# Kernel optimization log

Hardware: AMD Instinct MI355X
Metric: run time of the kernel (lower is better)

## Reference

```python
import jax, jax.numpy as jnp
import numpy as np

D_MODEL = 768; D_KV = 64; H = 12; D_FF = 3072; L = 2
TP = 4; SP = 16; MT = 16; MS = 4
MASK_RATE = 0.2; EPS = 1e-6
B = 256; T = 64; F = 64
ST = (T // TP) * (F // SP)  # 64 tokens


def ln(x, s, b):
    mu = jnp.mean(x, -1, keepdims=True)
    var = jnp.mean(jnp.square(x - mu), -1, keepdims=True)
    return (x - mu) * jax.lax.rsqrt(var + EPS) * s + b


def mha(x, Wq, bq, Wk, bk, Wv, bv, Wo, bo):
    Bz, S, D = x.shape
    q = (x @ Wq + bq).reshape(Bz, S, H, D_KV)
    k = (x @ Wk + bk).reshape(Bz, S, H, D_KV)
    v = (x @ Wv + bv).reshape(Bz, S, H, D_KV)
    scores = jnp.einsum('bqhd,bkhd->bhqk', q, k) * (D_KV ** -0.5)
    attn = jax.nn.softmax(scores, axis=-1)
    o = jnp.einsum('bhqk,bkhd->bqhd', attn, v).reshape(Bz, S, H * D_KV)
    return o @ Wo + bo


def setup_inputs():
    key = jax.random.key(0)
    ks = jax.random.split(key, 16)
    s = 0.02
    nrm = lambda k, shp: jax.random.normal(k, shp, jnp.float32) * s
    return {
        'inputs': jax.random.normal(ks[0], (B, T, F, 1), jnp.float32),
        'randomness': jax.random.uniform(ks[1], (B * ST, 3), jnp.float32),
        'perm': jax.random.permutation(ks[2], B * ST),
        'conv_w': nrm(ks[3], (TP, SP, 1, D_MODEL)), 'conv_b': jnp.zeros((D_MODEL,)),
        'temp_embd': nrm(ks[4], (MT, D_MODEL)), 'spec_embd': nrm(ks[5], (MS, D_MODEL)),
        'pos_ln_s': jnp.ones((D_MODEL,)), 'pos_ln_b': jnp.zeros((D_MODEL,)),
        'mask_tok': nrm(ks[6], (D_MODEL,)), 'agg_tok': nrm(ks[7], (D_MODEL,)),
        'Wq': nrm(ks[8], (L, D_MODEL, H * D_KV)), 'bq': jnp.zeros((L, H * D_KV)),
        'Wk': nrm(ks[9], (L, D_MODEL, H * D_KV)), 'bk': jnp.zeros((L, H * D_KV)),
        'Wv': nrm(ks[10], (L, D_MODEL, H * D_KV)), 'bv': jnp.zeros((L, H * D_KV)),
        'Wo': nrm(ks[11], (L, H * D_KV, D_MODEL)), 'bo': jnp.zeros((L, D_MODEL)),
        'ln1_s': jnp.ones((L, D_MODEL)), 'ln1_b': jnp.zeros((L, D_MODEL)),
        'W1': nrm(ks[12], (L, D_MODEL, D_FF)), 'b1': jnp.zeros((L, D_FF)),
        'W2': nrm(ks[13], (L, D_FF, D_MODEL)), 'b2': jnp.zeros((L, D_MODEL)),
        'ln2_s': jnp.ones((L, D_MODEL)), 'ln2_b': jnp.zeros((L, D_MODEL)),
    }


def reference(inputs, randomness, perm, conv_w, conv_b, temp_embd, spec_embd,
              pos_ln_s, pos_ln_b, mask_tok, agg_tok, Wq, bq, Wk, bk, Wv, bv,
              Wo, bo, ln1_s, ln1_b, W1, b1, W2, b2, ln2_s, ln2_b):
    # Conv2D patchify: [B, T, F, 1] -> [B, T/4, F/16, d_model]
    x = jax.lax.conv_general_dilated(
        inputs, conv_w, (TP, SP), 'VALID',
        dimension_numbers=('NHWC', 'HWIO', 'NHWC')) + conv_b
    Bz, Tt, Ss, D = x.shape
    e = x.reshape(Bz, Tt * Ss, D)  # token embeddings [B, 64, 768]
    # Vectorized BERT-style random masking (replaces the per-element sparse-scatter loop)
    sel = randomness[:, 0] <= MASK_RATE
    m = (sel & (randomness[:, 1] <= 0.8)).astype(e.dtype).reshape(Bz, Tt * Ss)
    rnd = (sel & (randomness[:, 1] > 0.8) & (randomness[:, 2] <= 0.5)).astype(e.dtype).reshape(Bz, Tt * Ss)
    shuffled = jax.lax.stop_gradient(e.reshape(-1, D))[perm].reshape(Bz, Tt * Ss, D)
    me = e * (1.0 - m - rnd)[..., None] + mask_tok * m[..., None] + shuffled * rnd[..., None]
    # Spectro-temporal position embeddings + LN
    pos = (temp_embd[:Tt, None, :] + spec_embd[None, :Ss, :]).reshape(Tt * Ss, D)
    h = ln(me + pos, pos_ln_s, pos_ln_b)
    # Prepend AGG token
    h = jnp.concatenate([jnp.broadcast_to(agg_tok, (Bz, 1, D)), h], axis=1)
    # Post-norm transformer encoder
    for l in range(L):
        a = mha(h, Wq[l], bq[l], Wk[l], bk[l], Wv[l], bv[l], Wo[l], bo[l])
        h = ln(h + a, ln1_s[l], ln1_b[l])
        f = jax.nn.gelu(h @ W1[l] + b1[l], approximate=False) @ W2[l] + b2[l]
        h = ln(h + f, ln2_s[l], ln2_b[l])
    return h  # last_hidden_states [B, 65, 768]; aggregated=h[:,0], predictions=h[:,1:]
```

## Files before the change

kernel.cpp:

```cpp
#include <hip/hip_runtime.h>
#include <hip/hip_bf16.h>
#include <math.h>

using bf16 = __hip_bfloat16;
typedef __bf16 bf16x8v __attribute__((ext_vector_type(8)));
typedef float f32x4 __attribute__((ext_vector_type(4)));
typedef unsigned short ushort4v __attribute__((ext_vector_type(4)));
typedef unsigned short ushort8v __attribute__((ext_vector_type(8)));

__device__ __forceinline__ float b2f(bf16 x) { return __bfloat162float(x); }
__device__ __forceinline__ bf16 f2b(float x) { return __float2bfloat16(x); }

__device__ __forceinline__ void gload_lds16(const void* g, void* l) {
  __builtin_amdgcn_global_load_lds(
      (__attribute__((address_space(1))) void*)(void*)g,
      (__attribute__((address_space(3))) void*)l, 16, 0, 0);
}

__device__ __forceinline__ float block_sum(float v, float* buf) {
  #pragma unroll
  for (int off = 32; off > 0; off >>= 1) v += __shfl_xor(v, off);
  __syncthreads();
  if ((threadIdx.x & 63) == 0) buf[threadIdx.x >> 6] = v;
  __syncthreads();
  return buf[0] + buf[1] + buf[2] + buf[3];
}

__global__ __launch_bounds__(256) void transpose_kernel(
    const float* __restrict__ in, bf16* __restrict__ out, int K, int N) {
  __shared__ float tile[32][33];
  const int nbx = N >> 5;
  const int bx = blockIdx.x % nbx, by = blockIdx.x / nbx;
  const int tx = threadIdx.x & 31, ty = threadIdx.x >> 5;
  #pragma unroll
  for (int i = 0; i < 4; ++i) {
    const int r = by * 32 + ty + i * 8;
    tile[ty + i * 8][tx] = in[(size_t)r * N + bx * 32 + tx];
  }
  __syncthreads();
  #pragma unroll
  for (int i = 0; i < 4; ++i) {
    const int r = bx * 32 + ty + i * 8;
    out[(size_t)r * K + by * 32 + tx] = f2b(tile[tx][ty + i * 8]);
  }
}

__global__ __launch_bounds__(256) void biasqkv_kernel(
    const float* __restrict__ bq, const float* __restrict__ bk,
    const float* __restrict__ bv, float* __restrict__ out) {
  const int i = blockIdx.x * 256 + threadIdx.x;
  if (i >= 2 * 2304) return;
  const int l = i / 2304, n = i % 2304;
  float v = (n < 768) ? bq[l * 768 + n]
          : (n < 1536) ? bk[l * 768 + n - 768] : bv[l * 768 + n - 1536];
  out[i] = v;
}

__global__ __launch_bounds__(256) void patchify_kernel(
    const float* __restrict__ in, const float* __restrict__ w,
    const float* __restrict__ cb, bf16* __restrict__ e) {
  __shared__ float patch[8][64];
  const int tid = threadIdx.x;
  const int tok0 = blockIdx.x * 8;
  for (int idx = tid; idx < 512; idx += 256) {
    const int t = idx >> 6, p = idx & 63;
    const int tok = tok0 + t;
    const int b = tok >> 6, t2 = tok & 63, tt = t2 >> 2, ss = t2 & 3;
    const int kt = p >> 4, kf = p & 15;
    patch[t][p] = in[((size_t)b * 64 + tt * 4 + kt) * 64 + ss * 16 + kf];
  }
  __syncthreads();
  for (int i = 0; i < 3; ++i) {
    const int d = tid + i * 256;
    const float cbv = cb[d];
    float acc[8];
    #pragma unroll
    for (int t = 0; t < 8; ++t) acc[t] = cbv;
    for (int p = 0; p < 64; ++p) {
      const float wv = w[p * 768 + d];
      #pragma unroll
      for (int t = 0; t < 8; ++t) acc[t] += patch[t][p] * wv;
    }
    #pragma unroll
    for (int t = 0; t < 8; ++t) e[(size_t)(tok0 + t) * 768 + d] = f2b(acc[t]);
  }
}

__global__ __launch_bounds__(256) void embed_kernel(
    const bf16* __restrict__ e, const float* __restrict__ randomness,
    const int* __restrict__ perm, const float* __restrict__ temp_embd,
    const float* __restrict__ spec_embd, const float* __restrict__ pls,
    const float* __restrict__ plb, const float* __restrict__ mask_tok,
    const float* __restrict__ agg_tok, bf16* __restrict__ h) {
  __shared__ float rbuf[4];
  const int row = blockIdx.x;
  const int b = row / 65, s = row % 65;
  const int tid = threadIdx.x;
  const size_t ob = (size_t)row * 768;
  if (s == 0) {
    #pragma unroll
    for (int i = 0; i < 3; ++i) { const int d = tid + i * 256; h[ob + d] = f2b(agg_tok[d]); }
    return;
  }
  const int tok = s - 1;
  const int gt = b * 64 + tok;
  const float r0 = randomness[gt * 3 + 0];
  const float r1 = randomness[gt * 3 + 1];
  const float r2 = randomness[gt * 3 + 2];
  const bool selb = (r0 <= 0.2f);
  const bool mflag = selb && (r1 <= 0.8f);
  const bool rflag = selb && (r1 > 0.8f) && (r2 <= 0.5f);
  const int src = rflag ? perm[gt] : gt;
  const int tt = tok >> 2, ss2 = tok & 3;
  float v[3]; float sum = 0.f;
  #pragma unroll
  for (int i = 0; i < 3; ++i) {
    const int d = tid + i * 256;
    const float ev = mflag ? mask_tok[d] : b2f(e[(size_t)src * 768 + d]);
    v[i] = ev + temp_embd[tt * 768 + d] + spec_embd[ss2 * 768 + d];
    sum += v[i];
  }
  const float mu = block_sum(sum, rbuf) * (1.f / 768.f);
  float q = 0.f;
  #pragma unroll
  for (int i = 0; i < 3; ++i) { const float t = v[i] - mu; q += t * t; }
  const float rstd = rsqrtf(block_sum(q, rbuf) * (1.f / 768.f) + 1e-6f);
  #pragma unroll
  for (int i = 0; i < 3; ++i) {
    const int d = tid + i * 256;
    h[ob + d] = f2b((v[i] - mu) * rstd * pls[d] + plb[d]);
  }
}

template <int F32OUT>
__global__ __launch_bounds__(256) void resln_kernel(
    const bf16* __restrict__ x, const bf16* __restrict__ y,
    const float* __restrict__ sc, const float* __restrict__ bi,
    void* __restrict__ outp) {
  __shared__ float rbuf[4];
  const int tid = threadIdx.x;
  const size_t base = (size_t)blockIdx.x * 768;
  float v[3]; float s = 0.f;
  #pragma unroll
  for (int i = 0; i < 3; ++i) {
    const int d = tid + i * 256;
    v[i] = b2f(x[base + d]) + b2f(y[base + d]);
    s += v[i];
  }
  const float mu = block_sum(s, rbuf) * (1.f / 768.f);
  float q = 0.f;
  #pragma unroll
  for (int i = 0; i < 3; ++i) { const float t = v[i] - mu; q += t * t; }
  const float rstd = rsqrtf(block_sum(q, rbuf) * (1.f / 768.f) + 1e-6f);
  #pragma unroll
  for (int i = 0; i < 3; ++i) {
    const int d = tid + i * 256;
    const float o = (v[i] - mu) * rstd * sc[d] + bi[d];
    if (F32OUT) ((float*)outp)[base + d] = o;
    else        ((bf16*)outp)[base + d] = f2b(o);
  }
}

template <int ACT>
__global__ __launch_bounds__(512, 2) void gemmkh_kernel(
    const unsigned short* __restrict__ A, const unsigned short* __restrict__ BT,
    const float* __restrict__ bias, bf16* __restrict__ C, int N, int K, int nbn) {
  __shared__ __align__(16) char smem[131072];

  const int nwg = gridDim.x;
  const int orig = blockIdx.x;
  const int q8 = nwg >> 3, r8 = nwg & 7;
  const int xcd = orig & 7, lin = orig >> 3;
  const int bid = (xcd < r8 ? xcd * (q8 + 1) : r8 * (q8 + 1) + (xcd - r8) * q8) + lin;
  const int bm = bid / nbn, bn = bid % nbn;

  const int tid = threadIdx.x;
  const int w = tid >> 6, lane = tid & 63;
  const int wrow = w >> 2, wcol = w & 3;
  const int frow = lane & 15;
  const int cg = lane >> 4;

  const size_t Kb = (size_t)K * 2;
  const int srow = lane >> 2;
  const int srcCB = (((lane & 3) ^ ((lane >> 3) & 3)) << 4);
  const char* gA = (const char*)A + ((size_t)bm * 256) * Kb;
  const char* gB = (const char*)BT + ((size_t)bn * 256) * Kb;

  f32x4 acc[8][4];
  #pragma unroll
  for (int i = 0; i < 8; ++i)
    #pragma unroll
    for (int j = 0; j < 4; ++j) acc[i][j] = f32x4{0.f, 0.f, 0.f, 0.f};

  auto stagePair = [&](int t, int h) {
    char* slot = smem + (size_t)(t & 1) * 65536;
    const size_t colb = (size_t)t * 128 + h * 64 + srcCB;
    #pragma unroll
    for (int j = 0; j < 2; ++j) {
      const int r = w * 32 + j * 16 + srow;
      gload_lds16(gA + (size_t)r * Kb + colb, slot + h * 16384 + w * 2048 + j * 1024);
      gload_lds16(gB + (size_t)r * Kb + colb, slot + 32768 + h * 16384 + w * 2048 + j * 1024);
    }
  };

  auto phase = [&](int t, int h) {
    const char* slot = smem + (size_t)(t & 1) * 65536;
    bf16x8v bb[4], aa[8];
    #pragma unroll
    for (int n = 0; n < 4; ++n) {
      const int row = wcol * 64 + n * 16 + frow;
      bb[n] = *(const bf16x8v*)(slot + 32768 + h * 16384 + row * 64 +
                                ((cg ^ ((row >> 1) & 3)) << 4));
    }
    #pragma unroll
    for (int m = 0; m < 8; ++m) {
      const int row = wrow * 128 + m * 16 + frow;
      aa[m] = *(const bf16x8v*)(slot + h * 16384 + row * 64 +
                                ((cg ^ ((row >> 1) & 3)) << 4));
    }
    __builtin_amdgcn_s_setprio(1);
    #pragma unroll
    for (int m = 0; m < 8; ++m)
      #pragma unroll
      for (int n = 0; n < 4; ++n)
        acc[m][n] = __builtin_amdgcn_mfma_f32_16x16x32_bf16(aa[m], bb[n], acc[m][n], 0, 0, 0);
    __builtin_amdgcn_s_setprio(0);
  };

  const int T = K >> 6;
  stagePair(0, 0);
  stagePair(0, 1);

  for (int t = 0; t < T - 1; ++t) {
    stagePair(t + 1, 0);
    asm volatile("s_waitcnt vmcnt(8)" ::: "memory");
    __builtin_amdgcn_s_barrier();
    __builtin_amdgcn_sched_barrier(0);
    phase(t, 0);
    stagePair(t + 1, 1);
    asm volatile("s_waitcnt vmcnt(8)" ::: "memory");
    __builtin_amdgcn_s_barrier();
    __builtin_amdgcn_sched_barrier(0);
    phase(t, 1);
  }
  asm volatile("s_waitcnt vmcnt(4)" ::: "memory");
  __builtin_amdgcn_s_barrier();
  __builtin_amdgcn_sched_barrier(0);
  phase(T - 1, 0);
  asm volatile("s_waitcnt vmcnt(0)" ::: "memory");
  __builtin_amdgcn_s_barrier();
  __builtin_amdgcn_sched_barrier(0);
  phase(T - 1, 1);
  __syncthreads();

  bf16* cbuf = (bf16*)smem;
  float bias4[4];
  #pragma unroll
  for (int n = 0; n < 4; ++n) bias4[n] = bias[bn * 256 + wcol * 64 + n * 16 + frow];
  const int rgrp = (lane >> 4) << 2;
  #pragma unroll
  for (int half = 0; half < 2; ++half) {
    if (wrow == half) {
      #pragma unroll
      for (int mf = 0; mf < 8; ++mf)
        #pragma unroll
        for (int n = 0; n < 4; ++n) {
          const int col = wcol * 64 + n * 16 + frow;
          #pragma unroll
          for (int r = 0; r < 4; ++r) {
            float v = acc[mf][n][r] + bias4[n];
            if (ACT == 1) v = 0.5f * v * (1.0f + erff(v * 0.70710678f));
            cbuf[(mf * 16 + rgrp + r) * 264 + col] = f2b(v);
          }
        }
    }
    __syncthreads();
    #pragma unroll
    for (int jj = 0; jj < 8; ++jj) {
      const int idx = tid + jj * 512;
      const int rowl = idx >> 5, c = idx & 31;
      const ushort8v val = *(const ushort8v*)(cbuf + rowl * 264 + c * 8);
      *(ushort8v*)(C + ((size_t)(bm * 256 + half * 128 + rowl)) * N + (size_t)bn * 256 + c * 8) = val;
    }
    __syncthreads();
  }
}

__global__ __launch_bounds__(320) void attn_mfma_kernel(
    const bf16* __restrict__ qkv, bf16* __restrict__ ctx) {
  __shared__ __align__(16) bf16 sK[80][72];
  __shared__ __align__(16) bf16 sVt[64][104];
  __shared__ __align__(16) bf16 sP[5][16][104];
  const int b = blockIdx.x / 12, h = blockIdx.x % 12;
  const int tid = threadIdx.x;
  const int wave = tid >> 6, lane = tid & 63;
  const size_t base = ((size_t)b * 65) * 2304 + (size_t)h * 64;
  const bf16 bzero = f2b(0.f);

  for (int idx = tid; idx < 65 * 16; idx += 320) {
    const int row = idx >> 4, d4 = (idx & 15) * 4;
    const ushort4v kv = *(const ushort4v*)(qkv + base + (size_t)row * 2304 + 768 + d4);
    const ushort4v vv = *(const ushort4v*)(qkv + base + (size_t)row * 2304 + 1536 + d4);
    *(ushort4v*)&sK[row][d4] = kv;
    #pragma unroll
    for (int j = 0; j < 4; ++j) ((unsigned short*)&sVt[d4 + j][row])[0] = vv[j];
  }
  for (int idx = tid; idx < 15 * 16; idx += 320) {
    const int row = 65 + (idx >> 4), d4 = (idx & 15) * 4;
    *(ushort4v*)&sK[row][d4] = ushort4v{0, 0, 0, 0};
  }
  for (int idx = tid; idx < 64 * 31; idx += 320) {
    const int d = idx / 31, c = 65 + (idx % 31);
    sVt[d][c] = bzero;
  }
  __syncthreads();

  const int frow = lane & 15;
  const int koff = (lane >> 4) * 8;
  const int row0 = wave * 16;
  const int qrow = (row0 + frow > 64) ? 64 : (row0 + frow);
  const bf16* qptr = qkv + base + (size_t)qrow * 2304;
  const bf16x8v aq0 = *(const bf16x8v*)(qptr + koff);
  const bf16x8v aq1 = *(const bf16x8v*)(qptr + 32 + koff);

  const f32x4 z4 = {0.f, 0.f, 0.f, 0.f};
  f32x4 sacc[5];
  #pragma unroll
  for (int n = 0; n < 5; ++n) sacc[n] = z4;
  #pragma unroll
  for (int n = 0; n < 5; ++n) {
    const bf16x8v b0 = *(const bf16x8v*)&sK[n * 16 + frow][koff];
    const bf16x8v b1 = *(const bf16x8v*)&sK[n * 16 + frow][32 + koff];
    sacc[n] = __builtin_amdgcn_mfma_f32_16x16x32_bf16(aq0, b0, sacc[n], 0, 0, 0);
    sacc[n] = __builtin_amdgcn_mfma_f32_16x16x32_bf16(aq1, b1, sacc[n], 0, 0, 0);
  }

  #pragma unroll
  for (int r = 0; r < 4; ++r) {
    const int prow = ((lane >> 4) << 2) + r;
    float v[5];
    float mx = -1e30f;
    #pragma unroll
    for (int n = 0; n < 5; ++n) {
      const int col = n * 16 + frow;
      v[n] = (col < 65) ? sacc[n][r] * 0.125f : -1e30f;
      mx = fmaxf(mx, v[n]);
    }
    #pragma unroll
    for (int off = 1; off < 16; off <<= 1) mx = fmaxf(mx, __shfl_xor(mx, off));
    float sum = 0.f;
    #pragma unroll
    for (int n = 0; n < 5; ++n) { v[n] = __expf(v[n] - mx); sum += v[n]; }
    #pragma unroll
    for (int off = 1; off < 16; off <<= 1) sum += __shfl_xor(sum, off);
    const float inv = 1.f / sum;
    #pragma unroll
    for (int n = 0; n < 5; ++n)
      sP[wave][prow][n * 16 + frow] = f2b(v[n] * inv);
    sP[wave][prow][80 + frow] = bzero;
  }

  f32x4 oacc[4];
  #pragma unroll
  for (int n = 0; n < 4; ++n) oacc[n] = z4;
  #pragma unroll
  for (int kk = 0; kk < 3; ++kk) {
    const bf16x8v ap = *(const bf16x8v*)&sP[wave][frow][kk * 32 + koff];
    #pragma unroll
    for (int n = 0; n < 4; ++n) {
      const bf16x8v bv = *(const bf16x8v*)&sVt[n * 16 + frow][kk * 32 + koff];
      oacc[n] = __builtin_amdgcn_mfma_f32_16x16x32_bf16(ap, bv, oacc[n], 0, 0, 0);
    }
  }

  #pragma unroll
  for (int r = 0; r < 4; ++r) {
    const int row = row0 + ((lane >> 4) << 2) + r;
    if (row < 65) {
      bf16* op = ctx + ((size_t)b * 65 + row) * 768 + (size_t)h * 64 + frow;
      #pragma unroll
      for (int n = 0; n < 4; ++n) op[n * 16] = f2b(oacc[n][r]);
    }
  }
}

extern "C" void kernel_launch(void* const* d_in, const int* in_sizes, int n_in,
                              void* d_out, int out_size, void* d_ws, size_t ws_size,
                              hipStream_t stream) {
  (void)in_sizes; (void)n_in; (void)out_size; (void)ws_size;
  const float* inputs     = (const float*)d_in[0];
  const float* randomness = (const float*)d_in[1];
  const int*   perm       = (const int*)d_in[2];
  const float* conv_w     = (const float*)d_in[3];
  const float* conv_b     = (const float*)d_in[4];
  const float* temp_embd  = (const float*)d_in[5];
  const float* spec_embd  = (const float*)d_in[6];
  const float* pos_ln_s   = (const float*)d_in[7];
  const float* pos_ln_b   = (const float*)d_in[8];
  const float* mask_tok   = (const float*)d_in[9];
  const float* agg_tok    = (const float*)d_in[10];
  const float* Wq = (const float*)d_in[11]; const float* bq = (const float*)d_in[12];
  const float* Wk = (const float*)d_in[13]; const float* bk = (const float*)d_in[14];
  const float* Wv = (const float*)d_in[15]; const float* bv = (const float*)d_in[16];
  const float* Wo = (const float*)d_in[17]; const float* bo = (const float*)d_in[18];
  const float* ln1_s = (const float*)d_in[19]; const float* ln1_b = (const float*)d_in[20];
  const float* W1 = (const float*)d_in[21]; const float* b1 = (const float*)d_in[22];
  const float* W2 = (const float*)d_in[23]; const float* b2 = (const float*)d_in[24];
  const float* ln2_s = (const float*)d_in[25]; const float* ln2_b = (const float*)d_in[26];

  char* wsb = (char*)d_ws;
  size_t off = 0;
  auto carve = [&](size_t bytes) { char* p = wsb + off; off = (off + bytes + 255) & ~(size_t)255; return p; };
  bf16* wqkvT = (bf16*)carve((size_t)2 * 2304 * 768 * 2);
  bf16* woT   = (bf16*)carve((size_t)2 * 768 * 768 * 2);
  bf16* w1T   = (bf16*)carve((size_t)2 * 3072 * 768 * 2);
  bf16* w2T   = (bf16*)carve((size_t)2 * 768 * 3072 * 2);
  float* bqkv = (float*)carve((size_t)2 * 2304 * 4);
  bf16* ebuf  = (bf16*)carve((size_t)16640 * 768 * 2);
  bf16* hbuf  = (bf16*)carve((size_t)16640 * 768 * 2);
  bf16* qkvb  = (bf16*)carve((size_t)16640 * 2304 * 2);
  bf16* ctxb  = (bf16*)carve((size_t)16640 * 768 * 2);
  bf16* tmpb  = ebuf;
  bf16* midb  = qkvb;

  const dim3 blk(256);
  for (int l = 0; l < 2; ++l) {
    transpose_kernel<<<576, blk, 0, stream>>>(Wq + (size_t)l * 768 * 768, wqkvT + (size_t)l * 2304 * 768, 768, 768);
    transpose_kernel<<<576, blk, 0, stream>>>(Wk + (size_t)l * 768 * 768, wqkvT + (size_t)l * 2304 * 768 + 768 * 768, 768, 768);
    transpose_kernel<<<576, blk, 0, stream>>>(Wv + (size_t)l * 768 * 768, wqkvT + (size_t)l * 2304 * 768 + 2 * 768 * 768, 768, 768);
    transpose_kernel<<<576, blk, 0, stream>>>(Wo + (size_t)l * 768 * 768, woT + (size_t)l * 768 * 768, 768, 768);
    transpose_kernel<<<2304, blk, 0, stream>>>(W1 + (size_t)l * 768 * 3072, w1T + (size_t)l * 3072 * 768, 768, 3072);
    transpose_kernel<<<2304, blk, 0, stream>>>(W2 + (size_t)l * 3072 * 768, w2T + (size_t)l * 768 * 3072, 3072, 768);
  }
  biasqkv_kernel<<<18, blk, 0, stream>>>(bq, bk, bv, bqkv);
  patchify_kernel<<<2048, blk, 0, stream>>>(inputs, conv_w, conv_b, ebuf);
  embed_kernel<<<16640, blk, 0, stream>>>(ebuf, randomness, perm, temp_embd, spec_embd,
                                          pos_ln_s, pos_ln_b, mask_tok, agg_tok, hbuf);
  for (int l = 0; l < 2; ++l) {
    gemmkh_kernel<0><<<65 * 9, dim3(512), 0, stream>>>(
        (const unsigned short*)hbuf, (const unsigned short*)(wqkvT + (size_t)l * 2304 * 768),
        bqkv + l * 2304, qkvb, 2304, 768, 9);
    attn_mfma_kernel<<<256 * 12, dim3(320), 0, stream>>>(qkvb, ctxb);
    gemmkh_kernel<0><<<65 * 3, dim3(512), 0, stream>>>(
        (const unsigned short*)ctxb, (const unsigned short*)(woT + (size_t)l * 768 * 768),
        bo + l * 768, tmpb, 768, 768, 3);
    resln_kernel<0><<<16640, blk, 0, stream>>>(hbuf, tmpb, ln1_s + l * 768, ln1_b + l * 768, hbuf);
    gemmkh_kernel<1><<<65 * 12, dim3(512), 0, stream>>>(
        (const unsigned short*)hbuf, (const unsigned short*)(w1T + (size_t)l * 3072 * 768),
        b1 + l * 3072, midb, 3072, 768, 12);
    gemmkh_kernel<0><<<65 * 3, dim3(512), 0, stream>>>(
        (const unsigned short*)midb, (const unsigned short*)(w2T + (size_t)l * 768 * 3072),
        b2 + l * 768, tmpb, 768, 3072, 3);
    if (l == 1)
      resln_kernel<1><<<16640, blk, 0, stream>>>(hbuf, tmpb, ln2_s + l * 768, ln2_b + l * 768, d_out);
    else
      resln_kernel<0><<<16640, blk, 0, stream>>>(hbuf, tmpb, ln2_s + l * 768, ln2_b + l * 768, hbuf);
  }
}
```

Baseline: 1.013 ms.

## Use triple-buffered K=32 GEMM pipeline and narrower N tiles for D_MODEL-output GEMMs

Replaces the double-buffered two-half-stage GEMM main loop with a three-slot ring buffer over K-steps of 32, prefetching two steps ahead behind a single barrier per step. It also adds a template option for 128-wide N tiles and uses it for the Wo and W2 projections, which doubles their grid from 195 to 390 workgroups. The aim is better latency hiding and better CU occupancy on the N=768 GEMMs. The cost is more barriers per unit of K, smaller per-barrier compute and lower arithmetic intensity for the narrow tiles.

```diff
diff --git a/kernel.cpp b/kernel.cpp
--- a/kernel.cpp
+++ b/kernel.cpp
@@ -161,11 +161,20 @@
   }
 }
 
-template <int ACT>
-__global__ __launch_bounds__(512, 2) void gemmkh_kernel(
+template <int WN, int ACT>
+__global__ __launch_bounds__(512, 2) void gemmp2_kernel(
     const unsigned short* __restrict__ A, const unsigned short* __restrict__ BT,
     const float* __restrict__ bias, bf16* __restrict__ C, int N, int K, int nbn) {
-  __shared__ __align__(16) char smem[131072];
+  constexpr int BN = 64 * WN;
+  constexpr int ABYTES = 256 * 64;
+  constexpr int BBYTES = BN * 64;
+  constexpr int SLOT = ABYTES + BBYTES;
+  constexpr int LPT = (256 + BN) / 128;
+  constexpr int MF = (WN == 4) ? 8 : 4;
+  constexpr int PADC = BN + 8;
+  constexpr int EPIB = (WN == 4) ? 128 * PADC * 2 : 256 * PADC * 2;
+  constexpr int SMEMB = (3 * SLOT > EPIB) ? 3 * SLOT : EPIB;
+  __shared__ __align__(16) char smem[SMEMB];
 
   const int nwg = gridDim.x;
   const int orig = blockIdx.x;
@@ -176,113 +185,131 @@
 
   const int tid = threadIdx.x;
   const int w = tid >> 6, lane = tid & 63;
-  const int wrow = w >> 2, wcol = w & 3;
+  const int wrow = (WN == 4) ? (w >> 2) : (w >> 1);
+  const int wcol = (WN == 4) ? (w & 3) : (w & 1);
   const int frow = lane & 15;
   const int cg = lane >> 4;
 
   const size_t Kb = (size_t)K * 2;
-  const int srow = lane >> 2;
+  const int g_lr = lane >> 2;
   const int srcCB = (((lane & 3) ^ ((lane >> 3) & 3)) << 4);
   const char* gA = (const char*)A + ((size_t)bm * 256) * Kb;
-  const char* gB = (const char*)BT + ((size_t)bn * 256) * Kb;
-
-  f32x4 acc[8][4];
-  #pragma unroll
-  for (int i = 0; i < 8; ++i)
+  const char* gB = (const char*)BT + ((size_t)bn * BN) * Kb;
+
+  f32x4 acc[MF][4];
+  #pragma unroll
+  for (int i = 0; i < MF; ++i)
     #pragma unroll
     for (int j = 0; j < 4; ++j) acc[i][j] = f32x4{0.f, 0.f, 0.f, 0.f};
 
-  auto stagePair = [&](int t, int h) {
-    char* slot = smem + (size_t)(t & 1) * 65536;
-    const size_t colb = (size_t)t * 128 + h * 64 + srcCB;
-    #pragma unroll
-    for (int j = 0; j < 2; ++j) {
-      const int r = w * 32 + j * 16 + srow;
-      gload_lds16(gA + (size_t)r * Kb + colb, slot + h * 16384 + w * 2048 + j * 1024);
-      gload_lds16(gB + (size_t)r * Kb + colb, slot + 32768 + h * 16384 + w * 2048 + j * 1024);
+  auto stage = [&](int t) {
+    char* slot = smem + (t % 3) * SLOT;
+    const size_t kb = (size_t)t * 64 + srcCB;
+    #pragma unroll
+    for (int g = 0; g < 2; ++g) {
+      const int r = g * 128 + w * 16 + g_lr;
+      gload_lds16(gA + (size_t)r * Kb + kb, slot + (g * 128 + w * 16) * 64);
+    }
+    #pragma unroll
+    for (int g = 0; g < LPT - 2; ++g) {
+      const int r = g * 128 + w * 16 + g_lr;
+      gload_lds16(gB + (size_t)r * Kb + kb, slot + ABYTES + (g * 128 + w * 16) * 64);
     }
   };
 
-  auto phase = [&](int t, int h) {
-    const char* slot = smem + (size_t)(t & 1) * 65536;
-    bf16x8v bb[4], aa[8];
+  auto compute = [&](int t) {
+    const char* slot = smem + (t % 3) * SLOT;
+    bf16x8v bb[4], aa[MF];
     #pragma unroll
     for (int n = 0; n < 4; ++n) {
       const int row = wcol * 64 + n * 16 + frow;
-      bb[n] = *(const bf16x8v*)(slot + 32768 + h * 16384 + row * 64 +
-                                ((cg ^ ((row >> 1) & 3)) << 4));
-    }
-    #pragma unroll
-    for (int m = 0; m < 8; ++m) {
-      const int row = wrow * 128 + m * 16 + frow;
-      aa[m] = *(const bf16x8v*)(slot + h * 16384 + row * 64 +
-                                ((cg ^ ((row >> 1) & 3)) << 4));
+      bb[n] = *(const bf16x8v*)(slot + ABYTES + row * 64 + ((cg ^ ((row >> 1) & 3)) << 4));
+    }
+    #pragma unroll
+    for (int m = 0; m < MF; ++m) {
+      const int row = wrow * (MF * 16) + m * 16 + frow;
+      aa[m] = *(const bf16x8v*)(slot + row * 64 + ((cg ^ ((row >> 1) & 3)) << 4));
     }
     __builtin_amdgcn_s_setprio(1);
     #pragma unroll
-    for (int m = 0; m < 8; ++m)
+    for (int m = 0; m < MF; ++m)
       #pragma unroll
       for (int n = 0; n < 4; ++n)
         acc[m][n] = __builtin_amdgcn_mfma_f32_16x16x32_bf16(aa[m], bb[n], acc[m][n], 0, 0, 0);
     __builtin_amdgcn_s_setprio(0);
   };
 
-  const int T = K >> 6;
-  stagePair(0, 0);
-  stagePair(0, 1);
-
-  for (int t = 0; t < T - 1; ++t) {
-    stagePair(t + 1, 0);
-    asm volatile("s_waitcnt vmcnt(8)" ::: "memory");
+  const int T = K >> 5;
+  stage(0);
+  stage(1);
+  for (int t = 0; t < T; ++t) {
+    if (t + 1 < T) {
+      if constexpr (WN == 4) asm volatile("s_waitcnt vmcnt(4)" ::: "memory");
+      else                   asm volatile("s_waitcnt vmcnt(3)" ::: "memory");
+    } else {
+      asm volatile("s_waitcnt vmcnt(0)" ::: "memory");
+    }
+    asm volatile("s_waitcnt lgkmcnt(0)" ::: "memory");
     __builtin_amdgcn_s_barrier();
     __builtin_amdgcn_sched_barrier(0);
-    phase(t, 0);
-    stagePair(t + 1, 1);
-    asm volatile("s_waitcnt vmcnt(8)" ::: "memory");
-    __builtin_amdgcn_s_barrier();
-    __builtin_amdgcn_sched_barrier(0);
-    phase(t, 1);
-  }
-  asm volatile("s_waitcnt vmcnt(4)" ::: "memory");
-  __builtin_amdgcn_s_barrier();
-  __builtin_amdgcn_sched_barrier(0);
-  phase(T - 1, 0);
-  asm volatile("s_waitcnt vmcnt(0)" ::: "memory");
-  __builtin_amdgcn_s_barrier();
-  __builtin_amdgcn_sched_barrier(0);
-  phase(T - 1, 1);
+    if (t + 2 < T) stage(t + 2);
+    compute(t);
+  }
   __syncthreads();
 
   bf16* cbuf = (bf16*)smem;
   float bias4[4];
   #pragma unroll
-  for (int n = 0; n < 4; ++n) bias4[n] = bias[bn * 256 + wcol * 64 + n * 16 + frow];
+  for (int n = 0; n < 4; ++n) bias4[n] = bias[bn * BN + wcol * 64 + n * 16 + frow];
   const int rgrp = (lane >> 4) << 2;
-  #pragma unroll
-  for (int half = 0; half < 2; ++half) {
-    if (wrow == half) {
+  if constexpr (WN == 4) {
+    #pragma unroll
+    for (int half = 0; half < 2; ++half) {
+      if (wrow == half) {
+        #pragma unroll
+        for (int mf = 0; mf < MF; ++mf)
+          #pragma unroll
+          for (int n = 0; n < 4; ++n) {
+            const int col = wcol * 64 + n * 16 + frow;
+            #pragma unroll
+            for (int r = 0; r < 4; ++r) {
+              float v = acc[mf][n][r] + bias4[n];
+              if (ACT == 1) v = 0.5f * v * (1.0f + erff(v * 0.70710678f));
+              cbuf[(mf * 16 + rgrp + r) * PADC + col] = f2b(v);
+            }
+          }
+      }
+      __syncthreads();
       #pragma unroll
-      for (int mf = 0; mf < 8; ++mf)
+      for (int jj = 0; jj < 8; ++jj) {
+        const int idx = tid + jj * 512;
+        const int rowl = idx >> 5, c = idx & 31;
+        const ushort8v val = *(const ushort8v*)(cbuf + rowl * PADC + c * 8);
+        *(ushort8v*)(C + ((size_t)(bm * 256 + half * 128 + rowl)) * N + (size_t)bn * BN + c * 8) = val;
+      }
+      __syncthreads();
+    }
+  } else {
+    #pragma unroll
+    for (int mf = 0; mf < MF; ++mf)
+      #pragma unroll
+      for (int n = 0; n < 4; ++n) {
+        const int col = wcol * 64 + n * 16 + frow;
         #pragma unroll
-        for (int n = 0; n < 4; ++n) {
-          const int col = wcol * 64 + n * 16 + frow;
-          #pragma unroll
-          for (int r = 0; r < 4; ++r) {
-            float v = acc[mf][n][r] + bias4[n];
-            if (ACT == 1) v = 0.5f * v * (1.0f + erff(v * 0.70710678f));
-            cbuf[(mf * 16 + rgrp + r) * 264 + col] = f2b(v);
-          }
+        for (int r = 0; r < 4; ++r) {
+          float v = acc[mf][n][r] + bias4[n];
+          if (ACT == 1) v = 0.5f * v * (1.0f + erff(v * 0.70710678f));
+          cbuf[(wrow * 64 + mf * 16 + rgrp + r) * PADC + col] = f2b(v);
         }
-    }
+      }
     __syncthreads();
     #pragma unroll
     for (int jj = 0; jj < 8; ++jj) {
       const int idx = tid + jj * 512;
-      const int rowl = idx >> 5, c = idx & 31;
-      const ushort8v val = *(const ushort8v*)(cbuf + rowl * 264 + c * 8);
-      *(ushort8v*)(C + ((size_t)(bm * 256 + half * 128 + rowl)) * N + (size_t)bn * 256 + c * 8) = val;
-    }
-    __syncthreads();
+      const int rowl = idx >> 4, c = idx & 15;
+      const ushort8v val = *(const ushort8v*)(cbuf + rowl * PADC + c * 8);
+      *(ushort8v*)(C + ((size_t)(bm * 256 + rowl)) * N + (size_t)bn * BN + c * 8) = val;
+    }
   }
 }
 
@@ -437,20 +464,20 @@
   embed_kernel<<<16640, blk, 0, stream>>>(ebuf, randomness, perm, temp_embd, spec_embd,
                                           pos_ln_s, pos_ln_b, mask_tok, agg_tok, hbuf);
   for (int l = 0; l < 2; ++l) {
-    gemmkh_kernel<0><<<65 * 9, dim3(512), 0, stream>>>(
+    gemmp2_kernel<4, 0><<<65 * 9, dim3(512), 0, stream>>>(
         (const unsigned short*)hbuf, (const unsigned short*)(wqkvT + (size_t)l * 2304 * 768),
         bqkv + l * 2304, qkvb, 2304, 768, 9);
     attn_mfma_kernel<<<256 * 12, dim3(320), 0, stream>>>(qkvb, ctxb);
-    gemmkh_kernel<0><<<65 * 3, dim3(512), 0, stream>>>(
+    gemmp2_kernel<2, 0><<<65 * 6, dim3(512), 0, stream>>>(
         (const unsigned short*)ctxb, (const unsigned short*)(woT + (size_t)l * 768 * 768),
-        bo + l * 768, tmpb, 768, 768, 3);
+        bo + l * 768, tmpb, 768, 768, 6);
     resln_kernel<0><<<16640, blk, 0, stream>>>(hbuf, tmpb, ln1_s + l * 768, ln1_b + l * 768, hbuf);
-    gemmkh_kernel<1><<<65 * 12, dim3(512), 0, stream>>>(
+    gemmp2_kernel<4, 1><<<65 * 12, dim3(512), 0, stream>>>(
         (const unsigned short*)hbuf, (const unsigned short*)(w1T + (size_t)l * 3072 * 768),
         b1 + l * 3072, midb, 3072, 768, 12);
-    gemmkh_kernel<0><<<65 * 3, dim3(512), 0, stream>>>(
+    gemmp2_kernel<2, 0><<<65 * 6, dim3(512), 0, stream>>>(
         (const unsigned short*)midb, (const unsigned short*)(w2T + (size_t)l * 768 * 3072),
-        b2 + l * 768, tmpb, 768, 3072, 3);
+        b2 + l * 768, tmpb, 768, 3072, 6);
     if (l == 1)
       resln_kernel<1><<<16640, blk, 0, stream>>>(hbuf, tmpb, ln2_s + l * 768, ln2_b + l * 768, d_out);
     else
```

Result: slower. 1.054 ms (+4.0%).

## Shrink GEMM tile to 256x128 with simple double buffer; merge weight transposes

Applied to the files above, without the earlier changes.

Replaces the 256x256 GEMM tile and its split-K pipelined staging with a 256x128 tile that stages one 32-wide K slice per iteration into a small double buffer. The kernel now uses 48KB of LDS and launch bounds of 4, so more workgroups can be resident and the grid is twice as large, which helps with tail and occupancy on small-N GEMMs. The cost is less reuse per tile, more barriers per K step, and giving up the hand-tuned vmcnt overlap. Separately, the twelve weight-transpose launches are merged into one kernel to cut launch overhead.

```diff
diff --git a/kernel.cpp b/kernel.cpp
--- a/kernel.cpp
+++ b/kernel.cpp
@@ -26,22 +26,44 @@
   return buf[0] + buf[1] + buf[2] + buf[3];
 }
 
-__global__ __launch_bounds__(256) void transpose_kernel(
-    const float* __restrict__ in, bf16* __restrict__ out, int K, int N) {
+__global__ __launch_bounds__(256) void transpose_all_kernel(
+    const float* __restrict__ Wq, const float* __restrict__ Wk,
+    const float* __restrict__ Wv, const float* __restrict__ Wo,
+    const float* __restrict__ W1, const float* __restrict__ W2,
+    bf16* __restrict__ wqkvT, bf16* __restrict__ woT,
+    bf16* __restrict__ w1T, bf16* __restrict__ w2T) {
   __shared__ float tile[32][33];
+  const int tb = blockIdx.x;
+  const float* src; bf16* dst; int K, N, t;
+  if (tb < 4608) {
+    const int job = tb / 576; t = tb % 576;
+    const int l = job >> 2, c = job & 3;
+    src = (c == 0 ? Wq : c == 1 ? Wk : c == 2 ? Wv : Wo) + (size_t)l * 768 * 768;
+    dst = (c < 3) ? (wqkvT + (size_t)l * 2304 * 768 + (size_t)c * 768 * 768)
+                  : (woT + (size_t)l * 768 * 768);
+    K = 768; N = 768;
+  } else if (tb < 9216) {
+    const int r = tb - 4608; const int l = r / 2304; t = r % 2304;
+    src = W1 + (size_t)l * 768 * 3072; dst = w1T + (size_t)l * 3072 * 768;
+    K = 768; N = 3072;
+  } else {
+    const int r = tb - 9216; const int l = r / 2304; t = r % 2304;
+    src = W2 + (size_t)l * 3072 * 768; dst = w2T + (size_t)l * 768 * 3072;
+    K = 3072; N = 768;
+  }
   const int nbx = N >> 5;
-  const int bx = blockIdx.x % nbx, by = blockIdx.x / nbx;
+  const int bx = t % nbx, by = t / nbx;
   const int tx = threadIdx.x & 31, ty = threadIdx.x >> 5;
   #pragma unroll
   for (int i = 0; i < 4; ++i) {
     const int r = by * 32 + ty + i * 8;
-    tile[ty + i * 8][tx] = in[(size_t)r * N + bx * 32 + tx];
+    tile[ty + i * 8][tx] = src[(size_t)r * N + bx * 32 + tx];
   }
   __syncthreads();
   #pragma unroll
   for (int i = 0; i < 4; ++i) {
     const int r = bx * 32 + ty + i * 8;
-    out[(size_t)r * K + by * 32 + tx] = f2b(tile[tx][ty + i * 8]);
+    dst[(size_t)r * K + by * 32 + tx] = f2b(tile[tx][ty + i * 8]);
   }
 }
 
@@ -162,10 +184,13 @@
 }
 
 template <int ACT>
-__global__ __launch_bounds__(512, 2) void gemmkh_kernel(
+__global__ __launch_bounds__(512, 4) void gemm2b_kernel(
     const unsigned short* __restrict__ A, const unsigned short* __restrict__ BT,
     const float* __restrict__ bias, bf16* __restrict__ C, int N, int K, int nbn) {
-  __shared__ __align__(16) char smem[131072];
+  constexpr int ABYTES = 256 * 64;
+  constexpr int BBYTES = 128 * 64;
+  constexpr int SLOT = ABYTES + BBYTES;
+  __shared__ __align__(16) char smem[2 * SLOT];
 
   const int nwg = gridDim.x;
   const int orig = blockIdx.x;
@@ -176,93 +201,79 @@
 
   const int tid = threadIdx.x;
   const int w = tid >> 6, lane = tid & 63;
-  const int wrow = w >> 2, wcol = w & 3;
+  const int wrow = w >> 1, wcol = w & 1;
   const int frow = lane & 15;
   const int cg = lane >> 4;
 
   const size_t Kb = (size_t)K * 2;
-  const int srow = lane >> 2;
+  const int g_lr = lane >> 2;
   const int srcCB = (((lane & 3) ^ ((lane >> 3) & 3)) << 4);
   const char* gA = (const char*)A + ((size_t)bm * 256) * Kb;
-  const char* gB = (const char*)BT + ((size_t)bn * 256) * Kb;
-
-  f32x4 acc[8][4];
-  #pragma unroll
-  for (int i = 0; i < 8; ++i)
+  const char* gB = (const char*)BT + ((size_t)bn * 128) * Kb;
+
+  f32x4 acc[4][4];
+  #pragma unroll
+  for (int i = 0; i < 4; ++i)
     #pragma unroll
     for (int j = 0; j < 4; ++j) acc[i][j] = f32x4{0.f, 0.f, 0.f, 0.f};
 
-  auto stagePair = [&](int t, int h) {
-    char* slot = smem + (size_t)(t & 1) * 65536;
-    const size_t colb = (size_t)t * 128 + h * 64 + srcCB;
+  auto stage = [&](int t, int slotIdx) {
+    char* slot = smem + slotIdx * SLOT;
+    const size_t kb = (size_t)t * 64 + srcCB;
     #pragma unroll
     for (int j = 0; j < 2; ++j) {
-      const int r = w * 32 + j * 16 + srow;
-      gload_lds16(gA + (size_t)r * Kb + colb, slot + h * 16384 + w * 2048 + j * 1024);
-      gload_lds16(gB + (size_t)r * Kb + colb, slot + 32768 + h * 16384 + w * 2048 + j * 1024);
+      const int r0 = w * 32 + j * 16;
+      gload_lds16(gA + (size_t)(r0 + g_lr) * Kb + kb, slot + r0 * 64);
+    }
+    {
+      const int r0 = w * 16;
+      gload_lds16(gB + (size_t)(r0 + g_lr) * Kb + kb, slot + ABYTES + r0 * 64);
     }
   };
 
-  auto phase = [&](int t, int h) {
-    const char* slot = smem + (size_t)(t & 1) * 65536;
-    bf16x8v bb[4], aa[8];
+  auto compute = [&](int slotIdx) {
+    const char* slot = smem + slotIdx * SLOT;
+    bf16x8v aa[4], bb[4];
     #pragma unroll
     for (int n = 0; n < 4; ++n) {
       const int row = wcol * 64 + n * 16 + frow;
-      bb[n] = *(const bf16x8v*)(slot + 32768 + h * 16384 + row * 64 +
-                                ((cg ^ ((row >> 1) & 3)) << 4));
-    }
-    #pragma unroll
-    for (int m = 0; m < 8; ++m) {
-      const int row = wrow * 128 + m * 16 + frow;
-      aa[m] = *(const bf16x8v*)(slot + h * 16384 + row * 64 +
-                                ((cg ^ ((row >> 1) & 3)) << 4));
+      bb[n] = *(const bf16x8v*)(slot + ABYTES + row * 64 + ((cg ^ ((row >> 1) & 3)) << 4));
+    }
+    #pragma unroll
+    for (int m = 0; m < 4; ++m) {
+      const int row = wrow * 64 + m * 16 + frow;
+      aa[m] = *(const bf16x8v*)(slot + row * 64 + ((cg ^ ((row >> 1) & 3)) << 4));
     }
     __builtin_amdgcn_s_setprio(1);
     #pragma unroll
-    for (int m = 0; m < 8; ++m)
+    for (int m = 0; m < 4; ++m)
       #pragma unroll
       for (int n = 0; n < 4; ++n)
         acc[m][n] = __builtin_amdgcn_mfma_f32_16x16x32_bf16(aa[m], bb[n], acc[m][n], 0, 0, 0);
     __builtin_amdgcn_s_setprio(0);
   };
 
-  const int T = K >> 6;
-  stagePair(0, 0);
-  stagePair(0, 1);
-
-  for (int t = 0; t < T - 1; ++t) {
-    stagePair(t + 1, 0);
-    asm volatile("s_waitcnt vmcnt(8)" ::: "memory");
-    __builtin_amdgcn_s_barrier();
-    __builtin_amdgcn_sched_barrier(0);
-    phase(t, 0);
-    stagePair(t + 1, 1);
-    asm volatile("s_waitcnt vmcnt(8)" ::: "memory");
-    __builtin_amdgcn_s_barrier();
-    __builtin_amdgcn_sched_barrier(0);
-    phase(t, 1);
-  }
-  asm volatile("s_waitcnt vmcnt(4)" ::: "memory");
-  __builtin_amdgcn_s_barrier();
-  __builtin_amdgcn_sched_barrier(0);
-  phase(T - 1, 0);
-  asm volatile("s_waitcnt vmcnt(0)" ::: "memory");
-  __builtin_amdgcn_s_barrier();
-  __builtin_amdgcn_sched_barrier(0);
-  phase(T - 1, 1);
-  __syncthreads();
+  const int T = K >> 5;
+  stage(0, 0);
+  __syncthreads();
+  int cur = 0;
+  for (int t = 0; t < T; ++t) {
+    if (t + 1 < T) stage(t + 1, cur ^ 1);
+    compute(cur);
+    __syncthreads();
+    cur ^= 1;
+  }
 
   bf16* cbuf = (bf16*)smem;
   float bias4[4];
   #pragma unroll
-  for (int n = 0; n < 4; ++n) bias4[n] = bias[bn * 256 + wcol * 64 + n * 16 + frow];
+  for (int n = 0; n < 4; ++n) bias4[n] = bias[bn * 128 + wcol * 64 + n * 16 + frow];
   const int rgrp = (lane >> 4) << 2;
   #pragma unroll
-  for (int half = 0; half < 2; ++half) {
-    if (wrow == half) {
+  for (int qtr = 0; qtr < 4; ++qtr) {
+    if (wrow == qtr) {
       #pragma unroll
-      for (int mf = 0; mf < 8; ++mf)
+      for (int mf = 0; mf < 4; ++mf)
         #pragma unroll
         for (int n = 0; n < 4; ++n) {
           const int col = wcol * 64 + n * 16 + frow;
@@ -270,17 +281,17 @@
           for (int r = 0; r < 4; ++r) {
             float v = acc[mf][n][r] + bias4[n];
             if (ACT == 1) v = 0.5f * v * (1.0f + erff(v * 0.70710678f));
-            cbuf[(mf * 16 + rgrp + r) * 264 + col] = f2b(v);
+            cbuf[(mf * 16 + rgrp + r) * 136 + col] = f2b(v);
           }
         }
     }
     __syncthreads();
     #pragma unroll
-    for (int jj = 0; jj < 8; ++jj) {
+    for (int jj = 0; jj < 2; ++jj) {
       const int idx = tid + jj * 512;
-      const int rowl = idx >> 5, c = idx & 31;
-      const ushort8v val = *(const ushort8v*)(cbuf + rowl * 264 + c * 8);
-      *(ushort8v*)(C + ((size_t)(bm * 256 + half * 128 + rowl)) * N + (size_t)bn * 256 + c * 8) = val;
+      const int rowl = idx >> 4, c = idx & 15;
+      const ushort8v val = *(const ushort8v*)(cbuf + rowl * 136 + c * 8);
+      *(ushort8v*)(C + ((size_t)(bm * 256 + qtr * 64 + rowl)) * N + (size_t)bn * 128 + c * 8) = val;
     }
     __syncthreads();
   }
@@ -424,33 +435,27 @@
   bf16* midb  = qkvb;
 
   const dim3 blk(256);
-  for (int l = 0; l < 2; ++l) {
-    transpose_kernel<<<576, blk, 0, stream>>>(Wq + (size_t)l * 768 * 768, wqkvT + (size_t)l * 2304 * 768, 768, 768);
-    transpose_kernel<<<576, blk, 0, stream>>>(Wk + (size_t)l * 768 * 768, wqkvT + (size_t)l * 2304 * 768 + 768 * 768, 768, 768);
-    transpose_kernel<<<576, blk, 0, stream>>>(Wv + (size_t)l * 768 * 768, wqkvT + (size_t)l * 2304 * 768 + 2 * 768 * 768, 768, 768);
-    transpose_kernel<<<576, blk, 0, stream>>>(Wo + (size_t)l * 768 * 768, woT + (size_t)l * 768 * 768, 768, 768);
-    transpose_kernel<<<2304, blk, 0, stream>>>(W1 + (size_t)l * 768 * 3072, w1T + (size_t)l * 3072 * 768, 768, 3072);
-    transpose_kernel<<<2304, blk, 0, stream>>>(W2 + (size_t)l * 3072 * 768, w2T + (size_t)l * 768 * 3072, 3072, 768);
-  }
+  transpose_all_kernel<<<13824, blk, 0, stream>>>(Wq, Wk, Wv, Wo, W1, W2,
+                                                  wqkvT, woT, w1T, w2T);
   biasqkv_kernel<<<18, blk, 0, stream>>>(bq, bk, bv, bqkv);
   patchify_kernel<<<2048, blk, 0, stream>>>(inputs, conv_w, conv_b, ebuf);
   embed_kernel<<<16640, blk, 0, stream>>>(ebuf, randomness, perm, temp_embd, spec_embd,
                                           pos_ln_s, pos_ln_b, mask_tok, agg_tok, hbuf);
   for (int l = 0; l < 2; ++l) {
-    gemmkh_kernel<0><<<65 * 9, dim3(512), 0, stream>>>(
+    gemm2b_kernel<0><<<65 * 18, dim3(512), 0, stream>>>(
         (const unsigned short*)hbuf, (const unsigned short*)(wqkvT + (size_t)l * 2304 * 768),
-        bqkv + l * 2304, qkvb, 2304, 768, 9);
+        bqkv + l * 2304, qkvb, 2304, 768, 18);
     attn_mfma_kernel<<<256 * 12, dim3(320), 0, stream>>>(qkvb, ctxb);
-    gemmkh_kernel<0><<<65 * 3, dim3(512), 0, stream>>>(
+    gemm2b_kernel<0><<<65 * 6, dim3(512), 0, stream>>>(
         (const unsigned short*)ctxb, (const unsigned short*)(woT + (size_t)l * 768 * 768),
-        bo + l * 768, tmpb, 768, 768, 3);
+        bo + l * 768, tmpb, 768, 768, 6);
     resln_kernel<0><<<16640, blk, 0, stream>>>(hbuf, tmpb, ln1_s + l * 768, ln1_b + l * 768, hbuf);
-    gemmkh_kernel<1><<<65 * 12, dim3(512), 0, stream>>>(
+    gemm2b_kernel<1><<<65 * 24, dim3(512), 0, stream>>>(
         (const unsigned short*)hbuf, (const unsigned short*)(w1T + (size_t)l * 3072 * 768),
-        b1 + l * 3072, midb, 3072, 768, 12);
-    gemmkh_kernel<0><<<65 * 3, dim3(512), 0, stream>>>(
+        b1 + l * 3072, midb, 3072, 768, 24);
+    gemm2b_kernel<0><<<65 * 6, dim3(512), 0, stream>>>(
         (const unsigned short*)midb, (const unsigned short*)(w2T + (size_t)l * 768 * 3072),
-        b2 + l * 768, tmpb, 768, 3072, 3);
+        b2 + l * 768, tmpb, 768, 3072, 6);
     if (l == 1)
       resln_kernel<1><<<16640, blk, 0, stream>>>(hbuf, tmpb, ln2_s + l * 768, ln2_b + l * 768, d_out);
     else
```

New measurement: 1.014 ms. No clear change (+0.0%).
